# Optimization experiments

Hardware: AMD Instinct MI355X
Metric: run time of the kernel (lower is better)

Reference implementation:

```python
import jax, jax.numpy as jnp
import numpy as np

B, LQ, LK, LS = 2, 2048, 2048, 256
HID, NH = 1024, 16
HD = HID // NH  # head_dim = 64


def setup_inputs() -> dict:
    key = jax.random.key(0)
    ks = jax.random.split(key, 14)
    s = 1.0 / np.sqrt(HID)
    inp = {
        "query": jax.random.normal(ks[0], (B, LQ, HID), jnp.float32),
        "sampled": jax.random.normal(ks[1], (B, LS, HID), jnp.float32),
        "key": jax.random.normal(ks[2], (B, LK, HID), jnp.float32),
        "value": jax.random.normal(ks[3], (B, LK, HID), jnp.float32),
        "Wq": jax.random.uniform(ks[4], (HID, HID), jnp.float32, -s, s),
        "bq": jax.random.uniform(ks[5], (HID,), jnp.float32, -s, s),
        "Wk": jax.random.uniform(ks[6], (HID, HID), jnp.float32, -s, s),
        "bk": jax.random.uniform(ks[7], (HID,), jnp.float32, -s, s),
        "Wv": jax.random.uniform(ks[8], (HID, HID), jnp.float32, -s, s),
        "bv": jax.random.uniform(ks[9], (HID,), jnp.float32, -s, s),
        "Wo": jax.random.uniform(ks[10], (HID, HID), jnp.float32, -s, s),
        "bo": jax.random.uniform(ks[11], (HID,), jnp.float32, -s, s),
        # fresh nn.Linear(LS+LK, LK) created each forward; fan_in = LS+LK
        "rW": jax.random.uniform(ks[12], (LK, LS + LK), jnp.float32, -1.0 / np.sqrt(LS + LK), 1.0 / np.sqrt(LS + LK)),
        "rb": jax.random.uniform(ks[13], (LK,), jnp.float32, -1.0 / np.sqrt(LS + LK), 1.0 / np.sqrt(LS + LK)),
    }
    return inp


def reference(query, sampled, key, value, Wq, bq, Wk, bk, Wv, bv, Wo, bo, rW, rb):
    scale = jnp.sqrt(jnp.float32(HD))
    Q = query @ Wq.T + bq                       # [B, LQ, HID]
    K = key @ Wk.T + bk                         # [B, LK, HID]
    V = value @ Wv.T + bv
    Kc = jnp.concatenate([sampled, K], axis=1)  # [B, LS+LK, HID]
    Vc = jnp.concatenate([sampled, V], axis=1)
    # seq-axis linear: out[b,t,h] = sum_s Kc[b,s,h] * rW[t,s] + rb[t]
    K = jnp.einsum("bsh,ts->bth", Kc, rW) + rb[None, :, None]  # [B, LK, HID]
    V = jnp.einsum("bsh,ts->bth", Vc, rW) + rb[None, :, None]
    # split heads: [B, NH, L, HD]
    Qh = Q.reshape(B, LQ, NH, HD).transpose(0, 2, 1, 3)
    Kh = K.reshape(B, LK, NH, HD).transpose(0, 2, 1, 3)
    Vh = V.reshape(B, LK, NH, HD).transpose(0, 2, 1, 3)
    energy = jnp.einsum("bhqd,bhkd->bhqk", Qh, Kh) / scale
    attention = jax.nn.softmax(energy, axis=-1)  # [B, NH, LQ, LK]
    x = jnp.einsum("bhqk,bhkd->bhqd", attention, Vh)
    x = x.transpose(0, 2, 1, 3).reshape(B, LQ, HID)
    x = x @ Wo.T + bo
    return x, attention
```

## Files before the change

### kernel.cpp

```cpp
#include <hip/hip_runtime.h>
#include <cstdint>
#include <cstddef>

#define NB   2
#define LQ   2048
#define LKK  2048
#define LS   256
#define HID  1024
#define NH   16
#define LSK  2304

#define DEV __device__ __forceinline__

typedef __bf16 bf16x8 __attribute__((ext_vector_type(8)));
typedef __bf16 bf16x4 __attribute__((ext_vector_type(4)));
typedef float  f32x4  __attribute__((ext_vector_type(4)));
typedef unsigned short us8 __attribute__((ext_vector_type(8)));

DEV unsigned short f2bf(float f) {
  unsigned int u = __builtin_bit_cast(unsigned int, f);
  u = (u + 0x7fffu + ((u >> 16) & 1u)) >> 16;
  return (unsigned short)u;
}
DEV bf16x8 ld_frag(const void* p) {
  uint4 v = *(const uint4*)p;
  return __builtin_bit_cast(bf16x8, v);
}
DEV void gload_lds16(const unsigned short* g, unsigned short* l) {
  __builtin_amdgcn_global_load_lds((const __attribute__((address_space(1))) unsigned int*)g,
                                   (__attribute__((address_space(3))) unsigned int*)l,
                                   16, 0, 0);
}

struct CastParams { const float* src[8]; unsigned short* dst[8]; int end8[8]; int total8; };

__global__ __launch_bounds__(256)
void cast_all(CastParams p) {
  const int stride = gridDim.x * blockDim.x;
  for (int i = blockIdx.x * blockDim.x + threadIdx.x; i < p.total8; i += stride) {
    int s = 0;
    while (i >= p.end8[s]) ++s;
    int base = s ? p.end8[s - 1] : 0;
    size_t off = (size_t)(i - base) * 8;
    const float4* q = (const float4*)(p.src[s] + off);
    float4 a = q[0], b = q[1];
    us8 o;
    o[0] = f2bf(a.x); o[1] = f2bf(a.y); o[2] = f2bf(a.z); o[3] = f2bf(a.w);
    o[4] = f2bf(b.x); o[5] = f2bf(b.y); o[6] = f2bf(b.z); o[7] = f2bf(b.w);
    *(us8*)(p.dst[s] + off) = o;
  }
}

__global__ __launch_bounds__(256)
void samp_T(const float* __restrict__ samp, unsigned short* __restrict__ KcT,
            unsigned short* __restrict__ VcT) {
  __shared__ unsigned short tl[64][65];
  const int b = blockIdx.z, st = blockIdx.x, nt = blockIdx.y;
  const int tid = threadIdx.x;
  const int nl = tid & 63, sq = tid >> 6;
#pragma unroll
  for (int j = 0; j < 16; ++j) {
    int sl = sq * 16 + j;
    tl[sl][nl] = f2bf(samp[(size_t)(b * LS + st * 64 + sl) * HID + nt * 64 + nl]);
  }
  __syncthreads();
#pragma unroll
  for (int wv = 0; wv < 2; ++wv) {
    int idx = wv * 256 + tid;
    int n_local = idx >> 3, sc = idx & 7;
    us8 v;
#pragma unroll
    for (int j = 0; j < 8; ++j) v[j] = tl[sc * 8 + j][n_local];
    size_t o = (size_t)(b * HID + nt * 64 + n_local) * LSK + st * 64 + sc * 8;
    *(us8*)(KcT + o) = v;
    *(us8*)(VcT + o) = v;
  }
}

struct GDesc {
  const unsigned short* A;
  const unsigned short* BT;
  const float* bias;
  void* out;
  int ldo, moff, K, flags;
  float oscale;
};
struct GParams { GDesc d[6]; int gxys; int chunk; };

__global__ __launch_bounds__(256, 2)
void gemm_multi(GParams p) {
  __shared__ unsigned short lA[128 * 64];
  __shared__ unsigned short lB[128 * 64];
  const int bid = blockIdx.x;
  const int wid = (bid & 7) * p.chunk + (bid >> 3);
  const int z = wid >> p.gxys;
  const int r = wid & ((1 << p.gxys) - 1);
  const int n0 = (r & 7) * 128, m0 = (r >> 3) * 128;
  const GDesc g = p.d[z];
  const int tid = threadIdx.x, l = tid & 63, w = tid >> 6;
  const int wr = w >> 1, wc = w & 1;
  const int K = g.K;
  const unsigned short* A = g.A;
  const unsigned short* BT = g.BT;
  f32x4 acc[4][4] = {};
  const int nk = K >> 6;
  for (int kt = 0; kt < nk; ++kt) {
    const int k0 = kt << 6;
#pragma unroll
    for (int it = 0; it < 4; ++it) {
      int s = it * 256 + tid;
      int t = s >> 3, c = s & 7, g2 = c ^ (t & 7);
      gload_lds16(A + (size_t)(m0 + t) * K + (k0 + g2 * 8), lA + (size_t)s * 8);
      gload_lds16(BT + (size_t)(n0 + t) * K + (k0 + g2 * 8), lB + (size_t)s * 8);
    }
    __syncthreads();
#pragma unroll
    for (int ks = 0; ks < 2; ++ks) {
      bf16x8 af[4], bfr[4];
#pragma unroll
      for (int mi = 0; mi < 4; ++mi) {
        int row = wr * 64 + mi * 16 + (l & 15);
        int ch = (ks * 4 + (l >> 4)) ^ (row & 7);
        af[mi] = ld_frag((const char*)lA + row * 128 + ch * 16);
      }
#pragma unroll
      for (int ni = 0; ni < 4; ++ni) {
        int row = wc * 64 + ni * 16 + (l & 15);
        int ch = (ks * 4 + (l >> 4)) ^ (row & 7);
        bfr[ni] = ld_frag((const char*)lB + row * 128 + ch * 16);
      }
#pragma unroll
      for (int mi = 0; mi < 4; ++mi)
#pragma unroll
        for (int ni = 0; ni < 4; ++ni)
          acc[mi][ni] = __builtin_amdgcn_mfma_f32_16x16x32_bf16(af[mi], bfr[ni], acc[mi][ni], 0, 0, 0);
    }
    __syncthreads();
  }
  const int epi = g.flags & 15, brow = g.flags >> 4;
  const int r4 = (l >> 4) * 4;
#pragma unroll
  for (int mi = 0; mi < 4; ++mi) {
    const int mbase = m0 + wr * 64 + mi * 16 + r4;
#pragma unroll
    for (int ni = 0; ni < 4; ++ni) {
      const int n = n0 + wc * 64 + ni * 16 + (l & 15);
      f32x4 v = acc[mi][ni];
      if (brow) {
#pragma unroll
        for (int rr = 0; rr < 4; ++rr) v[rr] = (v[rr] + g.bias[mbase + rr]) * g.oscale;
      } else {
        const float bn = g.bias[n];
#pragma unroll
        for (int rr = 0; rr < 4; ++rr) v[rr] = (v[rr] + bn) * g.oscale;
      }
      if (epi == 0) {
        unsigned short* o = (unsigned short*)g.out;
#pragma unroll
        for (int rr = 0; rr < 4; ++rr) o[(size_t)(mbase + rr) * g.ldo + n] = f2bf(v[rr]);
      } else if (epi == 1) {
        unsigned short* o = (unsigned short*)g.out;
        ushort4 pk;
        pk.x = f2bf(v[0]); pk.y = f2bf(v[1]); pk.z = f2bf(v[2]); pk.w = f2bf(v[3]);
        *(ushort4*)(o + (size_t)n * g.ldo + g.moff + mbase) = pk;
      } else {
        float* o = (float*)g.out;
#pragma unroll
        for (int rr = 0; rr < 4; ++rr) o[(size_t)(mbase + rr) * g.ldo + n] = v[rr];
      }
    }
  }
}

__global__ __launch_bounds__(256, 2)
void attn_fused(const unsigned short* __restrict__ Qb, const unsigned short* __restrict__ Kn,
                const unsigned short* __restrict__ Vt, float* __restrict__ attn_out,
                unsigned short* __restrict__ xpre) {
  __shared__ unsigned short smem[24576];
  const int tid = threadIdx.x, l = tid & 63, w = tid >> 6;
  const int bid = blockIdx.x;
  const int wid = (bid & 7) * 64 + (bid >> 3);
  const int qt = wid & 15, bh = wid >> 4, b = bh >> 4, h = bh & 15;
  const unsigned short* Qg = Qb + (size_t)(b * LQ + qt * 128) * HID + h * 64;
  const unsigned short* Kg = Kn + (size_t)(b * LKK) * HID + h * 64;
  const unsigned short* Vg = Vt + ((size_t)b * HID + h * 64) * LKK;
  unsigned short* const lK0 = smem;
  unsigned short* const lK1 = smem + 4096;
  unsigned short* const lV0 = smem + 8192;
  unsigned short* const lV1 = smem + 12288;
  unsigned short* const bufA = smem;
  unsigned short* const bufB = smem + 8192;
  unsigned short* const lPw = smem + 16384 + w * 2048;

#pragma unroll
  for (int it = 0; it < 4; ++it) {
    int s = it * 256 + tid, t = s >> 3, c = s & 7, g2 = c ^ (t & 7);
    gload_lds16(Qg + (size_t)t * HID + g2 * 8, smem + (size_t)s * 8);
  }
  __syncthreads();
  bf16x8 qf[2][2];
#pragma unroll
  for (int qi = 0; qi < 2; ++qi)
#pragma unroll
    for (int ds = 0; ds < 2; ++ds) {
      int row = w * 32 + qi * 16 + (l & 15);
      int ch = (ds * 4 + (l >> 4)) ^ (row & 7);
      qf[qi][ds] = ld_frag((const char*)smem + row * 128 + ch * 16);
    }
  __syncthreads();

  auto stageK128 = [&](int kt, unsigned short* dst) {
#pragma unroll
    for (int it = 0; it < 4; ++it) {
      int s = it * 256 + tid, t = s >> 3, c = s & 7, g2 = c ^ (t & 7);
      gload_lds16(Kg + (size_t)(kt * 128 + t) * HID + g2 * 8, dst + (size_t)s * 8);
    }
  };
  auto stageK = [&](int kt, unsigned short* dst) {
#pragma unroll
    for (int it = 0; it < 2; ++it) {
      int s = it * 256 + tid, t = s >> 3, c = s & 7, g2 = c ^ (t & 7);
      gload_lds16(Kg + (size_t)(kt * 64 + t) * HID + g2 * 8, dst + (size_t)s * 8);
    }
  };
  auto stageV = [&](int kt, unsigned short* dst) {
#pragma unroll
    for (int it = 0; it < 2; ++it) {
      int s = it * 256 + tid, t = s >> 3, c = s & 7, g2 = c ^ (t & 7);
      gload_lds16(Vg + (size_t)t * LKK + kt * 64 + g2 * 8, dst + (size_t)s * 8);
    }
  };

  float sm[2] = { 0.0f, 0.0f };
  stageK128(0, bufA);
  __syncthreads();
  for (int kt = 0; kt < 16; ++kt) {
    if (kt < 15) stageK128(kt + 1, (kt & 1) ? bufA : bufB);
    const unsigned short* cK = (kt & 1) ? bufB : bufA;
#pragma unroll
    for (int half = 0; half < 2; ++half) {
      f32x4 e[4][2] = {};
      __builtin_amdgcn_s_setprio(1);
#pragma unroll
      for (int ds = 0; ds < 2; ++ds) {
        bf16x8 kf[4];
#pragma unroll
        for (int ki = 0; ki < 4; ++ki) {
          int row = half * 64 + ki * 16 + (l & 15);
          int ch = (ds * 4 + (l >> 4)) ^ (row & 7);
          kf[ki] = ld_frag((const char*)cK + row * 128 + ch * 16);
        }
#pragma unroll
        for (int ki = 0; ki < 4; ++ki)
#pragma unroll
          for (int qi = 0; qi < 2; ++qi)
            e[ki][qi] = __builtin_amdgcn_mfma_f32_16x16x32_bf16(kf[ki], qf[qi][ds], e[ki][qi], 0, 0, 0);
      }
      __builtin_amdgcn_s_setprio(0);
#pragma unroll
      for (int qi = 0; qi < 2; ++qi) {
        float s_ = 0.0f;
#pragma unroll
        for (int ki = 0; ki < 4; ++ki)
#pragma unroll
          for (int r = 0; r < 4; ++r) s_ += __expf(e[ki][qi][r]);
        sm[qi] += s_;
      }
    }
    __syncthreads();
  }
  float rinv[2];
#pragma unroll
  for (int qi = 0; qi < 2; ++qi) {
    float ss = sm[qi];
    ss += __shfl_xor(ss, 16, 64);
    ss += __shfl_xor(ss, 32, 64);
    rinv[qi] = 1.0f / ss;
  }

  stageK(0, lK0); stageV(0, lV0);
  asm volatile("s_waitcnt vmcnt(0)" ::: "memory");
  __builtin_amdgcn_s_barrier();
  f32x4 x[2][4] = {};
  float* attn_base = attn_out + ((size_t)bh * LQ + qt * 128 + w * 32) * LKK;
  for (int kt = 0; kt < 32; ++kt) {
    if (kt < 31) {
      stageK(kt + 1, (kt & 1) ? lK0 : lK1);
      stageV(kt + 1, (kt & 1) ? lV0 : lV1);
    }
    __builtin_amdgcn_sched_barrier(0);
    const unsigned short* cK = (kt & 1) ? lK1 : lK0;
    const unsigned short* cV = (kt & 1) ? lV1 : lV0;
    f32x4 e[4][2] = {};
    __builtin_amdgcn_s_setprio(1);
#pragma unroll
    for (int ds = 0; ds < 2; ++ds) {
      bf16x8 kf[4];
#pragma unroll
      for (int ki = 0; ki < 4; ++ki) {
        int row = ki * 16 + (l & 15);
        int ch = (ds * 4 + (l >> 4)) ^ (row & 7);
        kf[ki] = ld_frag((const char*)cK + row * 128 + ch * 16);
      }
#pragma unroll
      for (int ki = 0; ki < 4; ++ki)
#pragma unroll
        for (int qi = 0; qi < 2; ++qi)
          e[ki][qi] = __builtin_amdgcn_mfma_f32_16x16x32_bf16(kf[ki], qf[qi][ds], e[ki][qi], 0, 0, 0);
    }
    __builtin_amdgcn_s_setprio(0);
#pragma unroll
    for (int qi = 0; qi < 2; ++qi) {
      const int q = qi * 16 + (l & 15);
      float* arow = attn_base + (size_t)q * LKK + kt * 64 + ((l >> 4) << 2);
#pragma unroll
      for (int ki = 0; ki < 4; ++ki) {
        float p0 = __expf(e[ki][qi][0]) * rinv[qi];
        float p1 = __expf(e[ki][qi][1]) * rinv[qi];
        float p2 = __expf(e[ki][qi][2]) * rinv[qi];
        float p3 = __expf(e[ki][qi][3]) * rinv[qi];
        float4 st; st.x = p0; st.y = p1; st.z = p2; st.w = p3;
        *(float4*)(arow + ki * 16) = st;
        bf16x4 pk;
        pk[0] = (__bf16)p0; pk[1] = (__bf16)p1; pk[2] = (__bf16)p2; pk[3] = (__bf16)p3;
        int chv = (ki * 2 + (l >> 5)) ^ (q & 7);
        *(bf16x4*)(lPw + q * 64 + chv * 8 + ((l >> 4) & 1) * 4) = pk;
      }
    }
    asm volatile("s_waitcnt lgkmcnt(0)" ::: "memory");
    __builtin_amdgcn_s_setprio(1);
#pragma unroll
    for (int ks = 0; ks < 2; ++ks) {
      bf16x8 pa[2], vb[4];
#pragma unroll
      for (int qi = 0; qi < 2; ++qi) {
        int row = qi * 16 + (l & 15);
        int ch = (ks * 4 + (l >> 4)) ^ (row & 7);
        pa[qi] = ld_frag((const char*)lPw + row * 128 + ch * 16);
      }
#pragma unroll
      for (int df = 0; df < 4; ++df) {
        int row = df * 16 + (l & 15);
        int ch = (ks * 4 + (l >> 4)) ^ (row & 7);
        vb[df] = ld_frag((const char*)cV + row * 128 + ch * 16);
      }
#pragma unroll
      for (int qi = 0; qi < 2; ++qi)
#pragma unroll
        for (int df = 0; df < 4; ++df)
          x[qi][df] = __builtin_amdgcn_mfma_f32_16x16x32_bf16(pa[qi], vb[df], x[qi][df], 0, 0, 0);
    }
    __builtin_amdgcn_s_setprio(0);
    asm volatile("s_waitcnt vmcnt(8)" ::: "memory");
    __builtin_amdgcn_s_barrier();
  }
#pragma unroll
  for (int qi = 0; qi < 2; ++qi)
#pragma unroll
    for (int df = 0; df < 4; ++df)
#pragma unroll
      for (int r = 0; r < 4; ++r)
        xpre[(size_t)(b * LQ + qt * 128 + w * 32 + qi * 16 + (l >> 4) * 4 + r) * HID
             + h * 64 + df * 16 + (l & 15)] = f2bf(x[qi][df][r]);
}

extern "C" void kernel_launch(void* const* d_in, const int* in_sizes, int n_in,
                              void* d_out, int out_size, void* d_ws, size_t ws_size,
                              hipStream_t stream) {
  (void)in_sizes; (void)n_in; (void)out_size; (void)ws_size;
  const float* query   = (const float*)d_in[0];
  const float* sampled = (const float*)d_in[1];
  const float* key     = (const float*)d_in[2];
  const float* value   = (const float*)d_in[3];
  const float* Wq = (const float*)d_in[4];  const float* bq = (const float*)d_in[5];
  const float* Wk = (const float*)d_in[6];  const float* bk = (const float*)d_in[7];
  const float* Wv = (const float*)d_in[8];  const float* bv = (const float*)d_in[9];
  const float* Wo = (const float*)d_in[10]; const float* bo = (const float*)d_in[11];
  const float* rW = (const float*)d_in[12]; const float* rb = (const float*)d_in[13];

  char* ws = (char*)d_ws;
  unsigned short* qb   = (unsigned short*)(ws + 0);
  unsigned short* keyb = (unsigned short*)(ws + 8388608);
  unsigned short* valb = (unsigned short*)(ws + 16777216);
  unsigned short* Wqb  = (unsigned short*)(ws + 25165824);
  unsigned short* Wkb  = (unsigned short*)(ws + 27262976);
  unsigned short* Wvb  = (unsigned short*)(ws + 29360128);
  unsigned short* Wob  = (unsigned short*)(ws + 31457280);
  unsigned short* rWb  = (unsigned short*)(ws + 33554432);
  unsigned short* Qbf  = (unsigned short*)(ws + 42991616);
  unsigned short* KcT  = (unsigned short*)(ws + 51380224);
  unsigned short* VcT  = (unsigned short*)(ws + 60817408);
  unsigned short* Knew = (unsigned short*)(ws + 70254592);
  unsigned short* Vt   = (unsigned short*)(ws + 78643200);
  unsigned short* xpre = (unsigned short*)(ws + 87031808);

  float* out_x    = (float*)d_out;
  float* out_attn = out_x + (size_t)NB * LQ * HID;

  CastParams cp;
  const float* srcs[8] = { query, key, value, Wq, Wk, Wv, Wo, rW };
  unsigned short* dsts[8] = { qb, keyb, valb, Wqb, Wkb, Wvb, Wob, rWb };
  const int sz8[8] = { 524288, 524288, 524288, 131072, 131072, 131072, 131072, 589824 };
  int acc = 0;
  for (int i = 0; i < 8; ++i) { cp.src[i] = srcs[i]; cp.dst[i] = dsts[i]; acc += sz8[i]; cp.end8[i] = acc; }
  cp.total8 = acc;
  cast_all<<<2048, 256, 0, stream>>>(cp);

  samp_T<<<dim3(4, 16, 2), 256, 0, stream>>>(sampled, KcT, VcT);

  GParams pp{};
  for (int b = 0; b < 2; ++b) {
    pp.d[b]     = { qb   + (size_t)b * 2048 * 1024, Wqb, bq, (void*)(Qbf + (size_t)b * 2048 * 1024),
                    1024, 0, 1024, 0, 0.125f };
    pp.d[2 + b] = { keyb + (size_t)b * 2048 * 1024, Wkb, bk, (void*)(KcT + (size_t)b * HID * LSK),
                    LSK, LS, 1024, 1, 1.0f };
    pp.d[4 + b] = { valb + (size_t)b * 2048 * 1024, Wvb, bv, (void*)(VcT + (size_t)b * HID * LSK),
                    LSK, LS, 1024, 1, 1.0f };
  }
  pp.gxys = 7; pp.chunk = 96;
  gemm_multi<<<768, 256, 0, stream>>>(pp);

  GParams sp{};
  for (int b = 0; b < 2; ++b) {
    sp.d[b]     = { rWb, KcT + (size_t)b * HID * LSK, rb, (void*)(Knew + (size_t)b * 2048 * 1024),
                    1024, 0, LSK, 0 | 16, 1.0f };
    sp.d[2 + b] = { rWb, VcT + (size_t)b * HID * LSK, rb, (void*)(Vt + (size_t)b * HID * LKK),
                    LKK, 0, LSK, 1 | 16, 1.0f };
  }
  sp.gxys = 7; sp.chunk = 64;
  gemm_multi<<<512, 256, 0, stream>>>(sp);

  attn_fused<<<512, 256, 0, stream>>>(Qbf, Knew, Vt, out_attn, xpre);

  GParams op{};
  op.d[0] = { xpre, Wob, bo, (void*)out_x, 1024, 0, 1024, 2, 1.0f };
  op.gxys = 8; op.chunk = 32;
  gemm_multi<<<256, 256, 0, stream>>>(op);
}
```

Baseline: 330.6 us.

## Fuse fp32 activation cast into GEMM loads, merge cast kernels, use exp2

Drops the separate bf16 cast of query/key/value. The projection GEMM now reads fp32 activations directly, converts them in registers and writes them to LDS, which removes a full write and re-read of the bf16 copies. The sampled transpose is merged into the weight-cast kernel to save one launch. Softmax now uses raw v_exp_f32 with the log2e factor folded into the Q scale. The fp32 A path uses synchronous register loads instead of async global-to-LDS loads and doubles the A bytes fetched per tile, which can slow the GEMM inner loop.

```diff
diff --git a/kernel.cpp b/kernel.cpp
--- a/kernel.cpp
+++ b/kernel.cpp
@@ -31,13 +31,40 @@
                                    (__attribute__((address_space(3))) unsigned int*)l,
                                    16, 0, 0);
 }
+DEV float fexp2(float x) { float r; asm("v_exp_f32 %0, %1" : "=v"(r) : "v"(x)); return r; }
 
 struct CastParams { const float* src[8]; unsigned short* dst[8]; int end8[8]; int total8; };
 
 __global__ __launch_bounds__(256)
-void cast_all(CastParams p) {
-  const int stride = gridDim.x * blockDim.x;
-  for (int i = blockIdx.x * blockDim.x + threadIdx.x; i < p.total8; i += stride) {
+void cast_samp(CastParams p, const float* __restrict__ samp,
+               unsigned short* __restrict__ KcT, unsigned short* __restrict__ VcT) {
+  __shared__ unsigned short tl[64][65];
+  const int tid = threadIdx.x;
+  if (blockIdx.x < 128) {
+    const int bid = blockIdx.x;
+    const int st = bid & 3, nt = (bid >> 2) & 15, b = bid >> 6;
+    const int nl = tid & 63, sq = tid >> 6;
+#pragma unroll
+    for (int j = 0; j < 16; ++j) {
+      int sl = sq * 16 + j;
+      tl[sl][nl] = f2bf(samp[(size_t)(b * LS + st * 64 + sl) * HID + nt * 64 + nl]);
+    }
+    __syncthreads();
+#pragma unroll
+    for (int wv = 0; wv < 2; ++wv) {
+      int idx = wv * 256 + tid;
+      int n_local = idx >> 3, sc = idx & 7;
+      us8 v;
+#pragma unroll
+      for (int j = 0; j < 8; ++j) v[j] = tl[sc * 8 + j][n_local];
+      size_t o = (size_t)(b * HID + nt * 64 + n_local) * LSK + st * 64 + sc * 8;
+      *(us8*)(KcT + o) = v;
+      *(us8*)(VcT + o) = v;
+    }
+    return;
+  }
+  const int stride = (gridDim.x - 128) * blockDim.x;
+  for (int i = (blockIdx.x - 128) * blockDim.x + tid; i < p.total8; i += stride) {
     int s = 0;
     while (i >= p.end8[s]) ++s;
     int base = s ? p.end8[s - 1] : 0;
@@ -51,34 +78,8 @@
   }
 }
 
-__global__ __launch_bounds__(256)
-void samp_T(const float* __restrict__ samp, unsigned short* __restrict__ KcT,
-            unsigned short* __restrict__ VcT) {
-  __shared__ unsigned short tl[64][65];
-  const int b = blockIdx.z, st = blockIdx.x, nt = blockIdx.y;
-  const int tid = threadIdx.x;
-  const int nl = tid & 63, sq = tid >> 6;
-#pragma unroll
-  for (int j = 0; j < 16; ++j) {
-    int sl = sq * 16 + j;
-    tl[sl][nl] = f2bf(samp[(size_t)(b * LS + st * 64 + sl) * HID + nt * 64 + nl]);
-  }
-  __syncthreads();
-#pragma unroll
-  for (int wv = 0; wv < 2; ++wv) {
-    int idx = wv * 256 + tid;
-    int n_local = idx >> 3, sc = idx & 7;
-    us8 v;
-#pragma unroll
-    for (int j = 0; j < 8; ++j) v[j] = tl[sc * 8 + j][n_local];
-    size_t o = (size_t)(b * HID + nt * 64 + n_local) * LSK + st * 64 + sc * 8;
-    *(us8*)(KcT + o) = v;
-    *(us8*)(VcT + o) = v;
-  }
-}
-
 struct GDesc {
-  const unsigned short* A;
+  const void* A;
   const unsigned short* BT;
   const float* bias;
   void* out;
@@ -100,18 +101,35 @@
   const int tid = threadIdx.x, l = tid & 63, w = tid >> 6;
   const int wr = w >> 1, wc = w & 1;
   const int K = g.K;
-  const unsigned short* A = g.A;
+  const int aF32 = (g.flags >> 5) & 1;
+  const unsigned short* A = (const unsigned short*)g.A;
+  const float* Af = (const float*)g.A;
   const unsigned short* BT = g.BT;
   f32x4 acc[4][4] = {};
   const int nk = K >> 6;
   for (int kt = 0; kt < nk; ++kt) {
     const int k0 = kt << 6;
-#pragma unroll
-    for (int it = 0; it < 4; ++it) {
-      int s = it * 256 + tid;
-      int t = s >> 3, c = s & 7, g2 = c ^ (t & 7);
-      gload_lds16(A + (size_t)(m0 + t) * K + (k0 + g2 * 8), lA + (size_t)s * 8);
-      gload_lds16(BT + (size_t)(n0 + t) * K + (k0 + g2 * 8), lB + (size_t)s * 8);
+    if (aF32) {
+#pragma unroll
+      for (int it = 0; it < 4; ++it) {
+        int s = it * 256 + tid;
+        int t = s >> 3, c = s & 7, g2 = c ^ (t & 7);
+        const float* src = Af + (size_t)(m0 + t) * K + (k0 + g2 * 8);
+        float4 u0 = *(const float4*)src, u1 = *(const float4*)(src + 4);
+        us8 o;
+        o[0] = f2bf(u0.x); o[1] = f2bf(u0.y); o[2] = f2bf(u0.z); o[3] = f2bf(u0.w);
+        o[4] = f2bf(u1.x); o[5] = f2bf(u1.y); o[6] = f2bf(u1.z); o[7] = f2bf(u1.w);
+        *(us8*)(lA + (size_t)s * 8) = o;
+        gload_lds16(BT + (size_t)(n0 + t) * K + (k0 + g2 * 8), lB + (size_t)s * 8);
+      }
+    } else {
+#pragma unroll
+      for (int it = 0; it < 4; ++it) {
+        int s = it * 256 + tid;
+        int t = s >> 3, c = s & 7, g2 = c ^ (t & 7);
+        gload_lds16(A + (size_t)(m0 + t) * K + (k0 + g2 * 8), lA + (size_t)s * 8);
+        gload_lds16(BT + (size_t)(n0 + t) * K + (k0 + g2 * 8), lB + (size_t)s * 8);
+      }
     }
     __syncthreads();
 #pragma unroll
@@ -137,7 +155,7 @@
     }
     __syncthreads();
   }
-  const int epi = g.flags & 15, brow = g.flags >> 4;
+  const int epi = g.flags & 15, brow = (g.flags >> 4) & 1;
   const int r4 = (l >> 4) * 4;
 #pragma unroll
   for (int mi = 0; mi < 4; ++mi) {
@@ -259,12 +277,15 @@
       __builtin_amdgcn_s_setprio(0);
 #pragma unroll
       for (int qi = 0; qi < 2; ++qi) {
-        float s_ = 0.0f;
-#pragma unroll
-        for (int ki = 0; ki < 4; ++ki)
-#pragma unroll
-          for (int r = 0; r < 4; ++r) s_ += __expf(e[ki][qi][r]);
-        sm[qi] += s_;
+        float s0 = 0.f, s1 = 0.f, s2 = 0.f, s3 = 0.f;
+#pragma unroll
+        for (int ki = 0; ki < 4; ++ki) {
+          s0 += fexp2(e[ki][qi][0]);
+          s1 += fexp2(e[ki][qi][1]);
+          s2 += fexp2(e[ki][qi][2]);
+          s3 += fexp2(e[ki][qi][3]);
+        }
+        sm[qi] += (s0 + s1) + (s2 + s3);
       }
     }
     __syncthreads();
@@ -315,10 +336,10 @@
       float* arow = attn_base + (size_t)q * LKK + kt * 64 + ((l >> 4) << 2);
 #pragma unroll
       for (int ki = 0; ki < 4; ++ki) {
-        float p0 = __expf(e[ki][qi][0]) * rinv[qi];
-        float p1 = __expf(e[ki][qi][1]) * rinv[qi];
-        float p2 = __expf(e[ki][qi][2]) * rinv[qi];
-        float p3 = __expf(e[ki][qi][3]) * rinv[qi];
+        float p0 = fexp2(e[ki][qi][0]) * rinv[qi];
+        float p1 = fexp2(e[ki][qi][1]) * rinv[qi];
+        float p2 = fexp2(e[ki][qi][2]) * rinv[qi];
+        float p3 = fexp2(e[ki][qi][3]) * rinv[qi];
         float4 st; st.x = p0; st.y = p1; st.z = p2; st.w = p3;
         *(float4*)(arow + ki * 16) = st;
         bf16x4 pk;
@@ -379,9 +400,6 @@
   const float* rW = (const float*)d_in[12]; const float* rb = (const float*)d_in[13];
 
   char* ws = (char*)d_ws;
-  unsigned short* qb   = (unsigned short*)(ws + 0);
-  unsigned short* keyb = (unsigned short*)(ws + 8388608);
-  unsigned short* valb = (unsigned short*)(ws + 16777216);
   unsigned short* Wqb  = (unsigned short*)(ws + 25165824);
   unsigned short* Wkb  = (unsigned short*)(ws + 27262976);
   unsigned short* Wvb  = (unsigned short*)(ws + 29360128);
@@ -397,35 +415,34 @@
   float* out_x    = (float*)d_out;
   float* out_attn = out_x + (size_t)NB * LQ * HID;
 
-  CastParams cp;
-  const float* srcs[8] = { query, key, value, Wq, Wk, Wv, Wo, rW };
-  unsigned short* dsts[8] = { qb, keyb, valb, Wqb, Wkb, Wvb, Wob, rWb };
-  const int sz8[8] = { 524288, 524288, 524288, 131072, 131072, 131072, 131072, 589824 };
+  CastParams cp{};
+  const float* srcs[5] = { Wq, Wk, Wv, Wo, rW };
+  unsigned short* dsts[5] = { Wqb, Wkb, Wvb, Wob, rWb };
+  const int sz8[5] = { 131072, 131072, 131072, 131072, 589824 };
   int acc = 0;
-  for (int i = 0; i < 8; ++i) { cp.src[i] = srcs[i]; cp.dst[i] = dsts[i]; acc += sz8[i]; cp.end8[i] = acc; }
+  for (int i = 0; i < 5; ++i) { cp.src[i] = srcs[i]; cp.dst[i] = dsts[i]; acc += sz8[i]; cp.end8[i] = acc; }
+  for (int i = 5; i < 8; ++i) { cp.src[i] = rW; cp.dst[i] = rWb; cp.end8[i] = 0x7fffffff; }
   cp.total8 = acc;
-  cast_all<<<2048, 256, 0, stream>>>(cp);
-
-  samp_T<<<dim3(4, 16, 2), 256, 0, stream>>>(sampled, KcT, VcT);
+  cast_samp<<<2176, 256, 0, stream>>>(cp, sampled, KcT, VcT);
 
   GParams pp{};
   for (int b = 0; b < 2; ++b) {
-    pp.d[b]     = { qb   + (size_t)b * 2048 * 1024, Wqb, bq, (void*)(Qbf + (size_t)b * 2048 * 1024),
-                    1024, 0, 1024, 0, 0.125f };
-    pp.d[2 + b] = { keyb + (size_t)b * 2048 * 1024, Wkb, bk, (void*)(KcT + (size_t)b * HID * LSK),
-                    LSK, LS, 1024, 1, 1.0f };
-    pp.d[4 + b] = { valb + (size_t)b * 2048 * 1024, Wvb, bv, (void*)(VcT + (size_t)b * HID * LSK),
-                    LSK, LS, 1024, 1, 1.0f };
+    pp.d[b]     = { (const void*)(query + (size_t)b * 2048 * 1024), Wqb, bq,
+                    (void*)(Qbf + (size_t)b * 2048 * 1024), 1024, 0, 1024, 0 | 32, 0.180336880f };
+    pp.d[2 + b] = { (const void*)(key + (size_t)b * 2048 * 1024), Wkb, bk,
+                    (void*)(KcT + (size_t)b * HID * LSK), LSK, LS, 1024, 1 | 32, 1.0f };
+    pp.d[4 + b] = { (const void*)(value + (size_t)b * 2048 * 1024), Wvb, bv,
+                    (void*)(VcT + (size_t)b * HID * LSK), LSK, LS, 1024, 1 | 32, 1.0f };
   }
   pp.gxys = 7; pp.chunk = 96;
   gemm_multi<<<768, 256, 0, stream>>>(pp);
 
   GParams sp{};
   for (int b = 0; b < 2; ++b) {
-    sp.d[b]     = { rWb, KcT + (size_t)b * HID * LSK, rb, (void*)(Knew + (size_t)b * 2048 * 1024),
-                    1024, 0, LSK, 0 | 16, 1.0f };
-    sp.d[2 + b] = { rWb, VcT + (size_t)b * HID * LSK, rb, (void*)(Vt + (size_t)b * HID * LKK),
-                    LKK, 0, LSK, 1 | 16, 1.0f };
+    sp.d[b]     = { (const void*)rWb, KcT + (size_t)b * HID * LSK, rb,
+                    (void*)(Knew + (size_t)b * 2048 * 1024), 1024, 0, LSK, 0 | 16, 1.0f };
+    sp.d[2 + b] = { (const void*)rWb, VcT + (size_t)b * HID * LSK, rb,
+                    (void*)(Vt + (size_t)b * HID * LKK), LKK, 0, LSK, 1 | 16, 1.0f };
   }
   sp.gxys = 7; sp.chunk = 64;
   gemm_multi<<<512, 256, 0, stream>>>(sp);
@@ -433,7 +450,7 @@
   attn_fused<<<512, 256, 0, stream>>>(Qbf, Knew, Vt, out_attn, xpre);
 
   GParams op{};
-  op.d[0] = { xpre, Wob, bo, (void*)out_x, 1024, 0, 1024, 2, 1.0f };
+  op.d[0] = { (const void*)xpre, Wob, bo, (void*)out_x, 1024, 0, 1024, 2, 1.0f };
   op.gxys = 8; op.chunk = 32;
   gemm_multi<<<256, 256, 0, stream>>>(op);
 }
```

New measurement: 335.0 us. Within noise of the previous version (+1.3%).
